# Kernel tuning notes

Measured on AMD Instinct MI355X. Metric: run time of the kernel, lower is better.

The kernel has to match this reference:

```python
import jax, jax.numpy as jnp
import numpy as np
from jax import lax

MINUS_INF = -1.0e9
BOS, EOS, PAD = 0, 1, 2
NB_LABELS, MAX_DEPTH, EXTRA = 96, 8, 3
STATE = NB_LABELS * MAX_DEPTH + EXTRA  # 771
B, T = 32, 128


def _init_transitions(key):
    t = jax.random.uniform(key, (STATE, STATE), minval=-0.1, maxval=0.1, dtype=jnp.float32)
    # structural constraints from init_weights()
    t = t.at[:, BOS].set(MINUS_INF)          # nothing transitions into BOS
    t = t.at[EOS, :].set(MINUS_INF)          # nothing leaves EOS
    t = t.at[BOS, NB_LABELS + EXTRA:].set(MINUS_INF)  # BOS only into depth-0 states
    t = t.at[NB_LABELS + EXTRA:, EOS].set(MINUS_INF)  # only depth-0 states into EOS
    t = t.at[PAD, :].set(MINUS_INF)
    t = t.at[NB_LABELS + EXTRA:, PAD].set(MINUS_INF)
    t = t.at[PAD, EOS].set(0.0)
    t = t.at[PAD, PAD].set(0.0)
    return t


def setup_inputs() -> dict:
    key = jax.random.key(0)
    k1, k2, k3 = jax.random.split(key, 3)
    emissions = jax.random.normal(k1, (B, T, STATE), dtype=jnp.float32)
    # valid (non-special) states only, so gold-path scores stay finite
    tags = jax.random.randint(k2, (B, T), EXTRA, STATE, dtype=jnp.int64)
    mask = jnp.ones((B, T), dtype=jnp.float32)
    transitions = _init_transitions(k3)
    return {"emissions": emissions, "tags": tags, "mask": mask, "transitions": transitions}


def _crf_nll(emissions, tags, mask, transitions):
    b, t, s = emissions.shape
    tags = tags.astype(jnp.int32)
    batch_idx = jnp.arange(b)

    # ---- gold path score ----
    first = tags[:, 0]
    scores = transitions[BOS, first] + emissions[batch_idx, 0, first]
    prev, cur = tags[:, :-1], tags[:, 1:]
    e_sc = jnp.take_along_axis(emissions[:, 1:], cur[..., None], axis=2)[..., 0]  # (B,T-1)
    t_sc = transitions[prev, cur]                                                 # (B,T-1)
    scores = scores + jnp.sum((e_sc + t_sc) * mask[:, 1:], axis=1)
    last_idx = mask.sum(axis=1).astype(jnp.int32) - 1
    last_tags = tags[batch_idx, last_idx]
    scores = scores + transitions[last_tags, EOS]

    # ---- log partition: forward algorithm (logsumexp DP over S x S) ----
    alphas0 = transitions[BOS][None, :] + emissions[:, 0]  # (B,S)

    def step(alphas, inp):
        em, m = inp  # em: (B,S), m: (B,)
        # (B,S_prev,1) + (S_prev,S_cur) + (B,1,S_cur) -> logsumexp over S_prev
        new = jax.scipy.special.logsumexp(
            alphas[:, :, None] + transitions[None, :, :] + em[:, None, :], axis=1)
        alphas = jnp.where(m[:, None] > 0, new, alphas)
        return alphas, None

    alphas, _ = lax.scan(step, alphas0,
                         (jnp.swapaxes(emissions[:, 1:], 0, 1), mask[:, 1:].T))
    log_z = jax.scipy.special.logsumexp(alphas + transitions[:, EOS][None, :], axis=1)

    # nll = -sum(score - logZ)
    return -jnp.sum(scores - log_z)


def reference(emissions, tags, mask, transitions):
    return _crf_nll(emissions, tags, mask, transitions)
```

## Files before the change

kernel.cpp:

```cpp
#include <hip/hip_runtime.h>
#include <math.h>

typedef unsigned long long u64;

static constexpr int S    = 771;
static constexpr int Tn   = 128;
static constexpr int Bn   = 32;
static constexpr int BOSs = 0;
static constexpr int EOSs = 1;

static constexpr int JPAD  = 832;
static constexpr int JB    = 13;
static constexpr int ROWS  = 64;
static constexpr int NQ    = 4;
static constexpr int SL    = JPAD / NQ;
static constexpr int CH    = SL / 16;
static constexpr int EBLK  = NQ * CH * ROWS * 16;
static constexpr int ETOT  = JB * EBLK;
static constexpr int XSTR  = 224;
static constexpr float CB  = 8.0f;
static constexpr float C0V = 4.5f;

__device__ __forceinline__ float wave_max_bfly(float v) {
    #pragma unroll
    for (int off = 32; off > 0; off >>= 1) v = fmaxf(v, __shfl_xor(v, off));
    return v;
}
__device__ __forceinline__ float wave_sum_f(float v) {
    #pragma unroll
    for (int off = 32; off > 0; off >>= 1) v += __shfl_down(v, off);
    return v;
}

__device__ __forceinline__ u64 ald64(const u64* p) {
    return __hip_atomic_load((u64*)p, __ATOMIC_RELAXED, __HIP_MEMORY_SCOPE_AGENT);
}
__device__ __forceinline__ void ast64(u64* p, u64 v) {
    __hip_atomic_store(p, v, __ATOMIC_RELAXED, __HIP_MEMORY_SCOPE_AGENT);
}
__device__ __forceinline__ u64 pack(unsigned tag, unsigned payload) {
    return ((u64)tag << 32) | (u64)payload;
}

#if __has_builtin(__builtin_amdgcn_sdot4)
__device__ __forceinline__ int dot4i(unsigned a, unsigned b, int c) {
    return __builtin_amdgcn_sdot4((int)a, (int)b, c, false);
}
#else
__device__ __forceinline__ int dot4i(unsigned a, unsigned b, int c) {
    c += (int)(a & 0xff)         * (int)(b & 0xff);
    c += (int)((a >> 8) & 0xff)  * (int)((b >> 8) & 0xff);
    c += (int)((a >> 16) & 0xff) * (int)((b >> 16) & 0xff);
    c += (int)((a >> 24) & 0xff) * (int)((b >> 24) & 0xff);
    return c;
}
#endif

extern "C" __global__ void build_tabs(const float* __restrict__ trans,
                                      unsigned char* __restrict__ eswz,
                                      float* __restrict__ eteos) {
    int idx = blockIdx.x * blockDim.x + threadIdx.x;
    if (idx < JPAD)
        eteos[idx] = (idx < S) ? __expf(trans[idx * S + EOSs]) : 0.f;
    if (idx >= ETOT) return;
    int e = idx & 15;
    int q = idx >> 4;
    int lane = q & 63;  q >>= 6;
    int kk = q % 13;
    int h  = q / 13;
    int w  = h & 3, jblk = h >> 2;
    int i = w * SL + kk * 16 + e;
    int j = jblk * ROWS + lane;
    float v = 0.f;
    if (i < S && j < S) v = 115.f * __expf(trans[i * S + j]);
    int q8 = (int)(v + 0.5f);
    if (q8 > 127) q8 = 127;
    eswz[idx] = (unsigned char)q8;
}

__device__ __forceinline__ void publish(u64* W, int jblk, unsigned tag,
                                        float af, float C, int lane) {
    float xf = fminf(127.f, 127.f * __expf(af - C));
    int xi = (int)(xf + 0.5f);
    int b0 = __shfl(xi, (4 * lane) & 63);
    int b1 = __shfl(xi, (4 * lane + 1) & 63);
    int b2 = __shfl(xi, (4 * lane + 2) & 63);
    int b3 = __shfl(xi, (4 * lane + 3) & 63);
    unsigned payload = (unsigned)b0 | ((unsigned)b1 << 8)
                     | ((unsigned)b2 << 16) | ((unsigned)b3 << 24);
    float mc = wave_max_bfly(af);
    u64* base = W + 17 * jblk;
    if (lane < 16)  ast64(base + lane, pack(tag, payload));
    if (lane == 16) ast64(base + 16,   pack(tag, __float_as_uint(mc)));
}

extern "C" __global__ __launch_bounds__(256, 2)
void crf_fwd(const float* __restrict__ em, const float* __restrict__ mask,
             const float* __restrict__ trans, const int* __restrict__ tags,
             const unsigned char* __restrict__ eswz,
             const float* __restrict__ eteos,
             u64* __restrict__ xb, float* __restrict__ out) {
    const int jblk = blockIdx.x, b = blockIdx.y;
    const int tid = threadIdx.x, lane = tid & 63, w = tid >> 6;
    const int j0 = jblk * ROWS;
    const int bw = (13 * w) / 4;
    const int lo = 52 * w - 16 * bw;

    __shared__ __align__(16) unsigned char Elds[EBLK];
    __shared__ __align__(16) unsigned pq[NQ][SL / 4];
    __shared__ int   part[2][NQ][ROWS];
    __shared__ float cshare;
    __shared__ float redv[4], redm[4];

    const float KLOG  = __logf(115.f * 127.f);
    const float KL127 = __logf(127.f);

    {
        const unsigned char* gsrc = eswz + (size_t)jblk * EBLK;
        #pragma unroll
        for (int it = 0; it < EBLK / 4096; ++it)
            *(float4*)(Elds + it * 4096 + tid * 16) =
                *(const float4*)(gsrc + it * 4096 + tid * 16);
    }

    float af = -INFINITY, Cuse = C0V;
    if (w == 0) {
        int j = j0 + lane;
        if (j < S) af = trans[BOSs * S + j] + em[((size_t)b * Tn + 0) * S + j];
        publish(xb + ((size_t)0 * Bn + b) * XSTR, jblk, 0u, af, C0V, lane);
    }

    const bool pollmax = (w == 0) && (lane < JB);

    for (int t = 1; t < Tn; ++t) {
        const u64* R = xb + ((size_t)((t - 1) & 1) * Bn + b) * XSTR;
        u64*       W = xb + ((size_t)((t    ) & 1) * Bn + b) * XSTR;

        float emv = 0.f, mval = 0.f;
        if (w == 0) {
            const int j = j0 + lane;
            if (j < S) emv = em[((size_t)b * Tn + t) * S + j];
            mval = mask[b * Tn + t];
        }

        const unsigned tg = (unsigned)(t - 1);
        const u64* pd = R + 17 * (bw + (lane >> 4)) + (lane & 15);
        const u64* pm = R + 17 * lane + 16;
        u64 qd = 0, qm = 0;
        bool okd = false, okm = !pollmax;
        do {
            if (!okd) { qd = ald64(pd); okd = ((unsigned)(qd >> 32) == tg); }
            if (!okm) { qm = ald64(pm); okm = ((unsigned)(qm >> 32) == tg); }
        } while (__any((!okd) | (!okm)));

        if (lane >= lo && lane < lo + 52) pq[w][lane - lo] = (unsigned)qd;

        float Cnew = 0.f;
        if (w == 0) {
            float mv = (lane < JB) ? __uint_as_float((unsigned)qm) : -INFINITY;
            Cnew = wave_max_bfly(mv) + CB;
        }

        int acc = 0;
        const uint4* E4 = (const uint4*)Elds;
        const uint4* P4 = (const uint4*)pq[w];
        #pragma unroll
        for (int kk = 0; kk < CH; ++kk) {
            const uint4 ev = E4[(w * CH + kk) * 64 + lane];
            const uint4 pv = P4[kk];
            acc = dot4i(ev.x, pv.x, acc);
            acc = dot4i(ev.y, pv.y, acc);
            acc = dot4i(ev.z, pv.z, acc);
            acc = dot4i(ev.w, pv.w, acc);
        }
        part[t & 1][w][lane] = acc;
        __syncthreads();

        if (w == 0) {
            int s4 = part[t & 1][0][lane] + part[t & 1][1][lane]
                   + part[t & 1][2][lane] + part[t & 1][3][lane];
            float nv = Cuse - KLOG + __logf((float)s4) + emv;
            af = (mval > 0.f) ? nv : af;
            publish(W, jblk, (unsigned)t, af, Cnew, lane);
            if (lane == 0) cshare = Cnew;
            Cuse = Cnew;
        }
    }

    if (jblk == 0) {
        const u64* R = xb + ((size_t)((Tn - 1) & 1) * Bn + b) * XSTR;
        const unsigned tg = (unsigned)(Tn - 1);
        const bool act = (tid < JB * 16);
        u64 q = 0;
        bool ok = !act;
        while (true) {
            if (!ok) {
                q = ald64(R + 17 * (tid >> 4) + (tid & 15));
                ok = ((unsigned)(q >> 32) == tg);
            }
            if (__syncthreads_and(ok)) break;
        }
        float lsum = 0.f;
        if (act) {
            unsigned pv = (unsigned)q;
            int base = 4 * tid;
            lsum = (float)(pv & 0xff)         * eteos[base]
                 + (float)((pv >> 8)  & 0xff) * eteos[base + 1]
                 + (float)((pv >> 16) & 0xff) * eteos[base + 2]
                 + (float)((pv >> 24) & 0xff) * eteos[base + 3];
        }
        float mk = 0.f, val = 0.f;
        if (tid < Tn) {
            mk = mask[b * Tn + tid];
            if (tid > 0) {
                int cur  = tags[b * Tn + tid];
                int prev = tags[b * Tn + tid - 1];
                val = (em[((size_t)b * Tn + tid) * S + cur]
                       + trans[prev * S + cur]) * mk;
            }
        }
        lsum = wave_sum_f(lsum);
        float vs = wave_sum_f(val);
        float ms = wave_sum_f(mk);
        if (lane == 0) { redv[w] = vs; redm[w] = ms; part[0][0][w] = 0; }
        if (lane == 1) part[1][0][w] = __float_as_int(lsum);
        __syncthreads();
        if (tid == 0) {
            float tot = __int_as_float(part[1][0][0]) + __int_as_float(part[1][0][1])
                      + __int_as_float(part[1][0][2]) + __int_as_float(part[1][0][3]);
            float logz = cshare - KL127 + __logf(tot);
            float msum = redm[0] + redm[1] + redm[2] + redm[3];
            int last   = (int)(msum + 0.5f) - 1;
            int first  = tags[b * Tn];
            int lastt  = tags[b * Tn + last];
            float score = redv[0] + redv[1] + redv[2] + redv[3]
                        + trans[BOSs * S + first]
                        + em[((size_t)b * Tn) * S + first]
                        + trans[lastt * S + EOSs];
            atomicAdd(out, -(score - logz));
        }
    }
}

extern "C" void kernel_launch(void* const* d_in, const int* in_sizes, int n_in,
                              void* d_out, int out_size, void* d_ws, size_t ws_size,
                              hipStream_t stream) {
    const float* em    = (const float*)d_in[0];
    const int*   tags  = (const int*)d_in[1];
    const float* mask  = (const float*)d_in[2];
    const float* trans = (const float*)d_in[3];
    float* out = (float*)d_out;

    char* ws = (char*)d_ws;
    size_t off = 0;
    unsigned char* eswz = (unsigned char*)(ws + off);
    off += (size_t)ETOT;
    off = (off + 255) & ~(size_t)255;
    float* eteos = (float*)(ws + off); off += JPAD * sizeof(float);
    off = (off + 255) & ~(size_t)255;
    u64* xb = (u64*)(ws + off);        off += (size_t)2 * Bn * XSTR * sizeof(u64);

    (void)hipMemsetAsync(out, 0, sizeof(float), stream);

    build_tabs<<<(ETOT + 255) / 256, 256, 0, stream>>>(trans, eswz, eteos);
    crf_fwd<<<dim3(JB, Bn), 256, 0, stream>>>(em, mask, trans, tags, eswz,
                                              eteos, xb, out);
}
```

Before: 391.0 us.

## Add L2-scoped fast polling path with epoch tags and XCD-aware block mapping

Publishes each step's quantized alpha payload twice: once with sc0 stores to a fast buffer meant to be polled through L2, and once with agent-scope atomics to a fallback buffer. Consumers spin on the fast buffer with sc0 loads up to a cap, then fall back to the coherent buffer for the rest of the run. Tags now carry a per-launch epoch read from s_memrealtime, so stale data from earlier launches cannot be mistaken for fresh data. Blocks are remapped from a 2D grid to a 1D index so that the 13 blocks of one batch row share an XCD. The aim is lower cross-block handoff latency, at the cost of doubled stores, reliance on L2 coherence that only holds within one XCD, and a global epoch handshake at start.

After: 501.0 us. +28.1%, slower.

```diff
diff --git a/kernel.cpp b/kernel.cpp
--- a/kernel.cpp
+++ b/kernel.cpp
@@ -18,6 +18,7 @@
 static constexpr int EBLK  = NQ * CH * ROWS * 16;
 static constexpr int ETOT  = JB * EBLK;
 static constexpr int XSTR  = 224;
+static constexpr int CAP   = 512;
 static constexpr float CB  = 8.0f;
 static constexpr float C0V = 4.5f;
 
@@ -37,6 +38,17 @@
 }
 __device__ __forceinline__ void ast64(u64* p, u64 v) {
     __hip_atomic_store(p, v, __ATOMIC_RELAXED, __HIP_MEMORY_SCOPE_AGENT);
+}
+__device__ __forceinline__ void ld2_l2(const u64* p0, const u64* p1,
+                                       u64& a, u64& c) {
+    asm volatile("global_load_dwordx2 %0, %2, off sc0\n\t"
+                 "global_load_dwordx2 %1, %3, off sc0\n\t"
+                 "s_waitcnt vmcnt(0)"
+                 : "=&v"(a), "=&v"(c) : "v"(p0), "v"(p1) : "memory");
+}
+__device__ __forceinline__ void st_l2(u64* p, u64 v) {
+    asm volatile("global_store_dwordx2 %0, %1, off sc0"
+                 :: "v"(p), "v"(v) : "memory");
 }
 __device__ __forceinline__ u64 pack(unsigned tag, unsigned payload) {
     return ((u64)tag << 32) | (u64)payload;
@@ -78,8 +90,9 @@
     eswz[idx] = (unsigned char)q8;
 }
 
-__device__ __forceinline__ void publish(u64* W, int jblk, unsigned tag,
-                                        float af, float C, int lane) {
+__device__ __forceinline__ void publish2(u64* WF, u64* WM, int jblk,
+                                         unsigned tag, float af, float C,
+                                         int lane) {
     float xf = fminf(127.f, 127.f * __expf(af - C));
     int xi = (int)(xf + 0.5f);
     int b0 = __shfl(xi, (4 * lane) & 63);
@@ -89,9 +102,12 @@
     unsigned payload = (unsigned)b0 | ((unsigned)b1 << 8)
                      | ((unsigned)b2 << 16) | ((unsigned)b3 << 24);
     float mc = wave_max_bfly(af);
-    u64* base = W + 17 * jblk;
-    if (lane < 16)  ast64(base + lane, pack(tag, payload));
-    if (lane == 16) ast64(base + 16,   pack(tag, __float_as_uint(mc)));
+    u64 vd = pack(tag, payload);
+    u64 vm = pack(tag, __float_as_uint(mc));
+    u64* bF = WF + 17 * jblk;
+    u64* bM = WM + 17 * jblk;
+    if (lane < 16)  { st_l2(bF + lane, vd); ast64(bM + lane, vd); }
+    if (lane == 16) { st_l2(bF + 16, vm);   ast64(bM + 16, vm); }
 }
 
 extern "C" __global__ __launch_bounds__(256, 2)
@@ -99,8 +115,11 @@
              const float* __restrict__ trans, const int* __restrict__ tags,
              const unsigned char* __restrict__ eswz,
              const float* __restrict__ eteos,
-             u64* __restrict__ xb, float* __restrict__ out) {
-    const int jblk = blockIdx.x, b = blockIdx.y;
+             u64* __restrict__ xbF, u64* __restrict__ xbM,
+             unsigned* __restrict__ ctl, float* __restrict__ out) {
+    const int l = blockIdx.x;
+    const int b    = (l & 7) + 8 * ((l >> 3) / JB);
+    const int jblk = (l >> 3) % JB;
     const int tid = threadIdx.x, lane = tid & 63, w = tid >> 6;
     const int j0 = jblk * ROWS;
     const int bw = (13 * w) / 4;
@@ -111,6 +130,7 @@
     __shared__ int   part[2][NQ][ROWS];
     __shared__ float cshare;
     __shared__ float redv[4], redm[4];
+    __shared__ unsigned sh_ep;
 
     const float KLOG  = __logf(115.f * 127.f);
     const float KL127 = __logf(127.f);
@@ -123,18 +143,39 @@
                 *(const float4*)(gsrc + it * 4096 + tid * 16);
     }
 
+    if (l == 0 && tid == 0) {
+        u64 rt;
+        asm volatile("s_memrealtime %0\n\ts_waitcnt lgkmcnt(0)" : "=s"(rt));
+        unsigned ep = ((unsigned)rt & 0xffffff00u) | 1u;
+        __hip_atomic_store(ctl, ep, __ATOMIC_RELAXED, __HIP_MEMORY_SCOPE_AGENT);
+    }
+    if (tid == 0) {
+        unsigned ev;
+        do {
+            ev = __hip_atomic_load(ctl, __ATOMIC_RELAXED,
+                                   __HIP_MEMORY_SCOPE_AGENT);
+        } while (!(ev & 1u));
+        sh_ep = ev;
+    }
+    __syncthreads();
+    const unsigned epoch = sh_ep;
+
     float af = -INFINITY, Cuse = C0V;
     if (w == 0) {
         int j = j0 + lane;
         if (j < S) af = trans[BOSs * S + j] + em[((size_t)b * Tn + 0) * S + j];
-        publish(xb + ((size_t)0 * Bn + b) * XSTR, jblk, 0u, af, C0V, lane);
+        publish2(xbF + ((size_t)0 * Bn + b) * XSTR,
+                 xbM + ((size_t)0 * Bn + b) * XSTR, jblk, epoch, af, C0V, lane);
     }
 
     const bool pollmax = (w == 0) && (lane < JB);
+    bool tryfast = true;
 
     for (int t = 1; t < Tn; ++t) {
-        const u64* R = xb + ((size_t)((t - 1) & 1) * Bn + b) * XSTR;
-        u64*       W = xb + ((size_t)((t    ) & 1) * Bn + b) * XSTR;
+        const size_t ro = ((size_t)((t - 1) & 1) * Bn + b) * XSTR;
+        const size_t wo = ((size_t)((t    ) & 1) * Bn + b) * XSTR;
+        const u64* RF = xbF + ro;
+        const u64* RM = xbM + ro;
 
         float emv = 0.f, mval = 0.f;
         if (w == 0) {
@@ -143,15 +184,32 @@
             mval = mask[b * Tn + t];
         }
 
-        const unsigned tg = (unsigned)(t - 1);
-        const u64* pd = R + 17 * (bw + (lane >> 4)) + (lane & 15);
-        const u64* pm = R + 17 * lane + 16;
+        const unsigned tg = epoch + (unsigned)(t - 1);
+        const int doff = 17 * (bw + (lane >> 4)) + (lane & 15);
+        const int moff = 17 * (pollmax ? lane : 0) + 16;
         u64 qd = 0, qm = 0;
         bool okd = false, okm = !pollmax;
-        do {
-            if (!okd) { qd = ald64(pd); okd = ((unsigned)(qd >> 32) == tg); }
-            if (!okm) { qm = ald64(pm); okm = ((unsigned)(qm >> 32) == tg); }
-        } while (__any((!okd) | (!okm)));
+        if (tryfast) {
+            const u64* pdF = RF + doff;
+            const u64* pmF = RF + moff;
+            int spins = 0;
+            for (;;) {
+                u64 a, c;
+                ld2_l2(pdF, pmF, a, c);
+                if (!okd) { qd = a; okd = ((unsigned)(qd >> 32) == tg); }
+                if (!okm) { qm = c; okm = ((unsigned)(qm >> 32) == tg); }
+                if (!__any((!okd) | (!okm))) break;
+                if (++spins >= CAP) { tryfast = false; break; }
+            }
+        }
+        if (__any((!okd) | (!okm))) {
+            const u64* pdM = RM + doff;
+            const u64* pmM = RM + moff;
+            do {
+                if (!okd) { qd = ald64(pdM); okd = ((unsigned)(qd >> 32) == tg); }
+                if (!okm) { qm = ald64(pmM); okm = ((unsigned)(qm >> 32) == tg); }
+            } while (__any((!okd) | (!okm)));
+        }
 
         if (lane >= lo && lane < lo + 52) pq[w][lane - lo] = (unsigned)qd;
 
@@ -181,23 +239,22 @@
                    + part[t & 1][2][lane] + part[t & 1][3][lane];
             float nv = Cuse - KLOG + __logf((float)s4) + emv;
             af = (mval > 0.f) ? nv : af;
-            publish(W, jblk, (unsigned)t, af, Cnew, lane);
+            publish2(xbF + wo, xbM + wo, jblk, epoch + (unsigned)t,
+                     af, Cnew, lane);
             if (lane == 0) cshare = Cnew;
             Cuse = Cnew;
         }
     }
 
     if (jblk == 0) {
-        const u64* R = xb + ((size_t)((Tn - 1) & 1) * Bn + b) * XSTR;
-        const unsigned tg = (unsigned)(Tn - 1);
+        const u64* R = xbM + ((size_t)((Tn - 1) & 1) * Bn + b) * XSTR;
+        const unsigned tg = epoch + (unsigned)(Tn - 1);
         const bool act = (tid < JB * 16);
+        const u64* pp = R + 17 * (tid >> 4) + (tid & 15);
         u64 q = 0;
         bool ok = !act;
         while (true) {
-            if (!ok) {
-                q = ald64(R + 17 * (tid >> 4) + (tid & 15));
-                ok = ((unsigned)(q >> 32) == tg);
-            }
+            if (!ok) { q = ald64(pp); ok = ((unsigned)(q >> 32) == tg); }
             if (__syncthreads_and(ok)) break;
         }
         float lsum = 0.f;
@@ -258,11 +315,15 @@
     off = (off + 255) & ~(size_t)255;
     float* eteos = (float*)(ws + off); off += JPAD * sizeof(float);
     off = (off + 255) & ~(size_t)255;
-    u64* xb = (u64*)(ws + off);        off += (size_t)2 * Bn * XSTR * sizeof(u64);
+    u64* xbF = (u64*)(ws + off);       off += (size_t)2 * Bn * XSTR * sizeof(u64);
+    off = (off + 255) & ~(size_t)255;
+    u64* xbM = (u64*)(ws + off);       off += (size_t)2 * Bn * XSTR * sizeof(u64);
+    off = (off + 255) & ~(size_t)255;
+    unsigned* ctl = (unsigned*)(ws + off); off += 256;
 
     (void)hipMemsetAsync(out, 0, sizeof(float), stream);
 
     build_tabs<<<(ETOT + 255) / 256, 256, 0, stream>>>(trans, eswz, eteos);
-    crf_fwd<<<dim3(JB, Bn), 256, 0, stream>>>(em, mask, trans, tags, eswz,
-                                              eteos, xb, out);
-}
+    crf_fwd<<<dim3(JB * Bn), 256, 0, stream>>>(em, mask, trans, tags, eswz,
+                                               eteos, xbF, xbM, ctl, out);
+}
```

## Process two batch rows per block and embed fp16 max in each published word

Applied to the files above, without the earlier changes.

Each workgroup now handles two sequences, interleaving their recurrence steps so one sequence's cross-block exchange latency can overlap the other's dot-product work. The grid is halved, so each block's LDS-resident quantized transition slice is reused for both sequences. The separate per-block max slot is removed: a half-precision running max and a 16-bit tag are packed into every published 64-bit word, so readers get the scale from the same load instead of an extra poll. The costs are reduced precision on the max (fp16), more serialized work per block, and the loss of the global-max poll being done by a single wave.

Result: slower. 435.4 us (+11.3%).

```diff
diff --git a/kernel.cpp b/kernel.cpp
--- a/kernel.cpp
+++ b/kernel.cpp
@@ -17,7 +17,9 @@
 static constexpr int CH    = SL / 16;
 static constexpr int EBLK  = NQ * CH * ROWS * 16;
 static constexpr int ETOT  = JB * EBLK;
+static constexpr int NPUB  = 16;
 static constexpr int XSTR  = 224;
+static constexpr unsigned TAGB = 0x5A00u;
 static constexpr float CB  = 8.0f;
 static constexpr float C0V = 4.5f;
 
@@ -32,14 +34,13 @@
     return v;
 }
 
+union HU16 { _Float16 h; unsigned short u; };
+
 __device__ __forceinline__ u64 ald64(const u64* p) {
     return __hip_atomic_load((u64*)p, __ATOMIC_RELAXED, __HIP_MEMORY_SCOPE_AGENT);
 }
 __device__ __forceinline__ void ast64(u64* p, u64 v) {
     __hip_atomic_store(p, v, __ATOMIC_RELAXED, __HIP_MEMORY_SCOPE_AGENT);
-}
-__device__ __forceinline__ u64 pack(unsigned tag, unsigned payload) {
-    return ((u64)tag << 32) | (u64)payload;
 }
 
 #if __has_builtin(__builtin_amdgcn_sdot4)
@@ -78,20 +79,20 @@
     eswz[idx] = (unsigned char)q8;
 }
 
-__device__ __forceinline__ void publish(u64* W, int jblk, unsigned tag,
-                                        float af, float C, int lane) {
+__device__ __forceinline__ void publish(u64* base, unsigned tg, float af,
+                                        float C, int lane) {
     float xf = fminf(127.f, 127.f * __expf(af - C));
     int xi = (int)(xf + 0.5f);
-    int b0 = __shfl(xi, (4 * lane) & 63);
-    int b1 = __shfl(xi, (4 * lane + 1) & 63);
-    int b2 = __shfl(xi, (4 * lane + 2) & 63);
-    int b3 = __shfl(xi, (4 * lane + 3) & 63);
-    unsigned payload = (unsigned)b0 | ((unsigned)b1 << 8)
-                     | ((unsigned)b2 << 16) | ((unsigned)b3 << 24);
+    int c0 = __shfl(xi, (4 * lane) & 63);
+    int c1 = __shfl(xi, (4 * lane + 1) & 63);
+    int c2 = __shfl(xi, (4 * lane + 2) & 63);
+    int c3 = __shfl(xi, (4 * lane + 3) & 63);
+    unsigned payload = (unsigned)c0 | ((unsigned)c1 << 8)
+                     | ((unsigned)c2 << 16) | ((unsigned)c3 << 24);
     float mc = wave_max_bfly(af);
-    u64* base = W + 17 * jblk;
-    if (lane < 16)  ast64(base + lane, pack(tag, payload));
-    if (lane == 16) ast64(base + 16,   pack(tag, __float_as_uint(mc)));
+    HU16 hh; hh.h = (_Float16)mc;
+    u64 v = ((u64)tg << 48) | ((u64)hh.u << 32) | (u64)payload;
+    if (lane < NPUB) ast64(base + lane, v);
 }
 
 extern "C" __global__ __launch_bounds__(256, 2)
@@ -100,16 +101,19 @@
              const unsigned char* __restrict__ eswz,
              const float* __restrict__ eteos,
              u64* __restrict__ xb, float* __restrict__ out) {
-    const int jblk = blockIdx.x, b = blockIdx.y;
+    const int jblk = blockIdx.x;
+    const int b0 = blockIdx.y * 2, b1 = b0 + 1;
     const int tid = threadIdx.x, lane = tid & 63, w = tid >> 6;
     const int j0 = jblk * ROWS;
     const int bw = (13 * w) / 4;
     const int lo = 52 * w - 16 * bw;
 
     __shared__ __align__(16) unsigned char Elds[EBLK];
-    __shared__ __align__(16) unsigned pq[NQ][SL / 4];
+    __shared__ __align__(16) unsigned pq[2][NQ][52];
     __shared__ int   part[2][NQ][ROWS];
-    __shared__ float cshare;
+    __shared__ float wmax[2][NQ];
+    __shared__ float csh[2];
+    __shared__ float lz[2][4];
     __shared__ float redv[4], redm[4];
 
     const float KLOG  = __logf(115.f * 127.f);
@@ -123,121 +127,159 @@
                 *(const float4*)(gsrc + it * 4096 + tid * 16);
     }
 
+    const int myb = (w == 1) ? b1 : b0;
     float af = -INFINITY, Cuse = C0V;
-    if (w == 0) {
+    if (w < 2) {
         int j = j0 + lane;
-        if (j < S) af = trans[BOSs * S + j] + em[((size_t)b * Tn + 0) * S + j];
-        publish(xb + ((size_t)0 * Bn + b) * XSTR, jblk, 0u, af, C0V, lane);
+        if (j < S) af = trans[BOSs * S + j] + em[((size_t)myb * Tn + 0) * S + j];
+        publish(xb + ((size_t)0 * Bn + myb) * XSTR + NPUB * jblk,
+                TAGB | 0u, af, C0V, lane);
     }
 
-    const bool pollmax = (w == 0) && (lane < JB);
-
     for (int t = 1; t < Tn; ++t) {
-        const u64* R = xb + ((size_t)((t - 1) & 1) * Bn + b) * XSTR;
-        u64*       W = xb + ((size_t)((t    ) & 1) * Bn + b) * XSTR;
+        const unsigned tgp = TAGB | (unsigned)(t - 1);
+        const unsigned tgc = TAGB | (unsigned)t;
 
         float emv = 0.f, mval = 0.f;
-        if (w == 0) {
+        if (w < 2) {
             const int j = j0 + lane;
-            if (j < S) emv = em[((size_t)b * Tn + t) * S + j];
-            mval = mask[b * Tn + t];
-        }
-
-        const unsigned tg = (unsigned)(t - 1);
-        const u64* pd = R + 17 * (bw + (lane >> 4)) + (lane & 15);
-        const u64* pm = R + 17 * lane + 16;
-        u64 qd = 0, qm = 0;
-        bool okd = false, okm = !pollmax;
-        do {
-            if (!okd) { qd = ald64(pd); okd = ((unsigned)(qd >> 32) == tg); }
-            if (!okm) { qm = ald64(pm); okm = ((unsigned)(qm >> 32) == tg); }
-        } while (__any((!okd) | (!okm)));
-
-        if (lane >= lo && lane < lo + 52) pq[w][lane - lo] = (unsigned)qd;
-
-        float Cnew = 0.f;
-        if (w == 0) {
-            float mv = (lane < JB) ? __uint_as_float((unsigned)qm) : -INFINITY;
-            Cnew = wave_max_bfly(mv) + CB;
-        }
-
-        int acc = 0;
-        const uint4* E4 = (const uint4*)Elds;
-        const uint4* P4 = (const uint4*)pq[w];
-        #pragma unroll
-        for (int kk = 0; kk < CH; ++kk) {
-            const uint4 ev = E4[(w * CH + kk) * 64 + lane];
-            const uint4 pv = P4[kk];
-            acc = dot4i(ev.x, pv.x, acc);
-            acc = dot4i(ev.y, pv.y, acc);
-            acc = dot4i(ev.z, pv.z, acc);
-            acc = dot4i(ev.w, pv.w, acc);
-        }
-        part[t & 1][w][lane] = acc;
-        __syncthreads();
-
-        if (w == 0) {
-            int s4 = part[t & 1][0][lane] + part[t & 1][1][lane]
-                   + part[t & 1][2][lane] + part[t & 1][3][lane];
-            float nv = Cuse - KLOG + __logf((float)s4) + emv;
-            af = (mval > 0.f) ? nv : af;
-            publish(W, jblk, (unsigned)t, af, Cnew, lane);
-            if (lane == 0) cshare = Cnew;
-            Cuse = Cnew;
+            if (j < S) emv = em[((size_t)myb * Tn + t) * S + j];
+            mval = mask[myb * Tn + t];
+        }
+
+        {
+            const u64* R = xb + ((size_t)((t - 1) & 1) * Bn + b0) * XSTR;
+            const u64* pd = R + NPUB * (bw + (lane >> 4)) + (lane & 15);
+            u64 q = 0; bool ok = false;
+            do {
+                if (!ok) { q = ald64(pd); ok = ((unsigned)(q >> 48) == tgp); }
+            } while (__any(!ok));
+            if (lane >= lo && lane < lo + 52) pq[0][w][lane - lo] = (unsigned)q;
+            HU16 hm; hm.u = (unsigned short)(q >> 32);
+            float wm = wave_max_bfly((float)hm.h);
+            if (lane == 0) wmax[0][w] = wm;
+
+            int acc = 0;
+            const uint4* E4 = (const uint4*)Elds;
+            const uint4* P4 = (const uint4*)pq[0][w];
+            #pragma unroll
+            for (int kk = 0; kk < CH; ++kk) {
+                const uint4 ev = E4[(w * CH + kk) * 64 + lane];
+                const uint4 pv = P4[kk];
+                acc = dot4i(ev.x, pv.x, acc); acc = dot4i(ev.y, pv.y, acc);
+                acc = dot4i(ev.z, pv.z, acc); acc = dot4i(ev.w, pv.w, acc);
+            }
+            part[0][w][lane] = acc;
+            __syncthreads();
+            if (w == 0) {
+                int s4 = part[0][0][lane] + part[0][1][lane]
+                       + part[0][2][lane] + part[0][3][lane];
+                float Cnew = fmaxf(fmaxf(wmax[0][0], wmax[0][1]),
+                                   fmaxf(wmax[0][2], wmax[0][3])) + CB;
+                float nv = Cuse - KLOG + __logf((float)s4) + emv;
+                af = (mval > 0.f) ? nv : af;
+                publish(xb + ((size_t)(t & 1) * Bn + b0) * XSTR + NPUB * jblk,
+                        tgc, af, Cnew, lane);
+                Cuse = Cnew;
+            }
+        }
+
+        {
+            const u64* R = xb + ((size_t)((t - 1) & 1) * Bn + b1) * XSTR;
+            const u64* pd = R + NPUB * (bw + (lane >> 4)) + (lane & 15);
+            u64 q = 0; bool ok = false;
+            do {
+                if (!ok) { q = ald64(pd); ok = ((unsigned)(q >> 48) == tgp); }
+            } while (__any(!ok));
+            if (lane >= lo && lane < lo + 52) pq[1][w][lane - lo] = (unsigned)q;
+            HU16 hm; hm.u = (unsigned short)(q >> 32);
+            float wm = wave_max_bfly((float)hm.h);
+            if (lane == 0) wmax[1][w] = wm;
+
+            int acc = 0;
+            const uint4* E4 = (const uint4*)Elds;
+            const uint4* P4 = (const uint4*)pq[1][w];
+            #pragma unroll
+            for (int kk = 0; kk < CH; ++kk) {
+                const uint4 ev = E4[(w * CH + kk) * 64 + lane];
+                const uint4 pv = P4[kk];
+                acc = dot4i(ev.x, pv.x, acc); acc = dot4i(ev.y, pv.y, acc);
+                acc = dot4i(ev.z, pv.z, acc); acc = dot4i(ev.w, pv.w, acc);
+            }
+            part[1][w][lane] = acc;
+            __syncthreads();
+            if (w == 1) {
+                int s4 = part[1][0][lane] + part[1][1][lane]
+                       + part[1][2][lane] + part[1][3][lane];
+                float Cnew = fmaxf(fmaxf(wmax[1][0], wmax[1][1]),
+                                   fmaxf(wmax[1][2], wmax[1][3])) + CB;
+                float nv = Cuse - KLOG + __logf((float)s4) + emv;
+                af = (mval > 0.f) ? nv : af;
+                publish(xb + ((size_t)(t & 1) * Bn + b1) * XSTR + NPUB * jblk,
+                        tgc, af, Cnew, lane);
+                Cuse = Cnew;
+            }
         }
     }
 
     if (jblk == 0) {
-        const u64* R = xb + ((size_t)((Tn - 1) & 1) * Bn + b) * XSTR;
-        const unsigned tg = (unsigned)(Tn - 1);
-        const bool act = (tid < JB * 16);
-        u64 q = 0;
-        bool ok = !act;
+        if (w < 2 && lane == 0) csh[w] = Cuse;
+        const unsigned tgf = TAGB | (unsigned)(Tn - 1);
+        const u64* RA = xb + ((size_t)((Tn - 1) & 1) * Bn + b0) * XSTR;
+        const u64* RB = xb + ((size_t)((Tn - 1) & 1) * Bn + b1) * XSTR;
+        const bool actp = (tid < JB * NPUB);
+        u64 qa = 0, qb = 0;
+        bool oka = !actp, okb = !actp;
         while (true) {
-            if (!ok) {
-                q = ald64(R + 17 * (tid >> 4) + (tid & 15));
-                ok = ((unsigned)(q >> 32) == tg);
-            }
-            if (__syncthreads_and(ok)) break;
-        }
-        float lsum = 0.f;
-        if (act) {
-            unsigned pv = (unsigned)q;
+            if (!oka) { qa = ald64(RA + tid); oka = ((unsigned)(qa >> 48) == tgf); }
+            if (!okb) { qb = ald64(RB + tid); okb = ((unsigned)(qb >> 48) == tgf); }
+            if (__syncthreads_and(oka & okb)) break;
+        }
+        float lA = 0.f, lB = 0.f;
+        if (actp) {
+            unsigned pa = (unsigned)qa, pb = (unsigned)qb;
             int base = 4 * tid;
-            lsum = (float)(pv & 0xff)         * eteos[base]
-                 + (float)((pv >> 8)  & 0xff) * eteos[base + 1]
-                 + (float)((pv >> 16) & 0xff) * eteos[base + 2]
-                 + (float)((pv >> 24) & 0xff) * eteos[base + 3];
-        }
-        float mk = 0.f, val = 0.f;
-        if (tid < Tn) {
-            mk = mask[b * Tn + tid];
-            if (tid > 0) {
-                int cur  = tags[b * Tn + tid];
-                int prev = tags[b * Tn + tid - 1];
-                val = (em[((size_t)b * Tn + tid) * S + cur]
-                       + trans[prev * S + cur]) * mk;
-            }
-        }
-        lsum = wave_sum_f(lsum);
+            lA = (float)(pa & 0xff)         * eteos[base]
+               + (float)((pa >> 8)  & 0xff) * eteos[base + 1]
+               + (float)((pa >> 16) & 0xff) * eteos[base + 2]
+               + (float)((pa >> 24) & 0xff) * eteos[base + 3];
+            lB = (float)(pb & 0xff)         * eteos[base]
+               + (float)((pb >> 8)  & 0xff) * eteos[base + 1]
+               + (float)((pb >> 16) & 0xff) * eteos[base + 2]
+               + (float)((pb >> 24) & 0xff) * eteos[base + 3];
+        }
+        lA = wave_sum_f(lA);
+        lB = wave_sum_f(lB);
+        if (lane == 0) { lz[0][w] = lA; lz[1][w] = lB; }
+
+        int pos = tid & 127;
+        int gb  = (tid < 128) ? b0 : b1;
+        float mk = mask[gb * Tn + pos];
+        float val = 0.f;
+        if (pos > 0) {
+            int cur  = tags[gb * Tn + pos];
+            int prev = tags[gb * Tn + pos - 1];
+            val = (em[((size_t)gb * Tn + pos) * S + cur]
+                   + trans[prev * S + cur]) * mk;
+        }
         float vs = wave_sum_f(val);
         float ms = wave_sum_f(mk);
-        if (lane == 0) { redv[w] = vs; redm[w] = ms; part[0][0][w] = 0; }
-        if (lane == 1) part[1][0][w] = __float_as_int(lsum);
+        if (lane == 0) { redv[w] = vs; redm[w] = ms; }
         __syncthreads();
         if (tid == 0) {
-            float tot = __int_as_float(part[1][0][0]) + __int_as_float(part[1][0][1])
-                      + __int_as_float(part[1][0][2]) + __int_as_float(part[1][0][3]);
-            float logz = cshare - KL127 + __logf(tot);
-            float msum = redm[0] + redm[1] + redm[2] + redm[3];
-            int last   = (int)(msum + 0.5f) - 1;
-            int first  = tags[b * Tn];
-            int lastt  = tags[b * Tn + last];
-            float score = redv[0] + redv[1] + redv[2] + redv[3]
-                        + trans[BOSs * S + first]
-                        + em[((size_t)b * Tn) * S + first]
-                        + trans[lastt * S + EOSs];
-            atomicAdd(out, -(score - logz));
+            float totA = lz[0][0] + lz[0][1] + lz[0][2] + lz[0][3];
+            float totB = lz[1][0] + lz[1][1] + lz[1][2] + lz[1][3];
+            float logzA = csh[0] - KL127 + __logf(totA);
+            float logzB = csh[1] - KL127 + __logf(totB);
+            float msA = redm[0] + redm[1], msB = redm[2] + redm[3];
+            int lastA = (int)(msA + 0.5f) - 1, lastB = (int)(msB + 0.5f) - 1;
+            int fA = tags[b0 * Tn], fB = tags[b1 * Tn];
+            int lTA = tags[b0 * Tn + lastA], lTB = tags[b1 * Tn + lastB];
+            float scoreA = redv[0] + redv[1] + trans[BOSs * S + fA]
+                         + em[((size_t)b0 * Tn) * S + fA] + trans[lTA * S + EOSs];
+            float scoreB = redv[2] + redv[3] + trans[BOSs * S + fB]
+                         + em[((size_t)b1 * Tn) * S + fB] + trans[lTB * S + EOSs];
+            atomicAdd(out, -(scoreA - logzA) - (scoreB - logzB));
         }
     }
 }
@@ -263,6 +305,6 @@
     (void)hipMemsetAsync(out, 0, sizeof(float), stream);
 
     build_tabs<<<(ETOT + 255) / 256, 256, 0, stream>>>(trans, eswz, eteos);
-    crf_fwd<<<dim3(JB, Bn), 256, 0, stream>>>(em, mask, trans, tags, eswz,
-                                              eteos, xb, out);
-}
+    crf_fwd<<<dim3(JB, Bn / 2), 256, 0, stream>>>(em, mask, trans, tags, eswz,
+                                                  eteos, xb, out);
+}
```

## Split rows across waves so each wave publishes independently without block barrier

Applied to the files above, without the earlier changes.

Reassigns work so each of the four waves owns 16 output rows and the full 832-column dot product, reduced with in-wave shuffles instead of an LDS partial-sum exchange and __syncthreads. Each wave now publishes its own 4-word slice with the per-slice max packed as fp16 alongside a 16-bit tag, so the separate max words and their polling disappear. The goal is to shorten the per-timestep critical path of the cross-block recurrence. In exchange every wave polls all 208 words, and the fp16 max and shorter tag lose some precision and range.

Measured after the change: 416.6 us. 1.07x slower.

```diff
diff --git a/kernel.cpp b/kernel.cpp
--- a/kernel.cpp
+++ b/kernel.cpp
@@ -11,13 +11,13 @@
 
 static constexpr int JPAD  = 832;
 static constexpr int JB    = 13;
-static constexpr int ROWS  = 64;
 static constexpr int NQ    = 4;
-static constexpr int SL    = JPAD / NQ;
-static constexpr int CH    = SL / 16;
-static constexpr int EBLK  = NQ * CH * ROWS * 16;
+static constexpr int CH    = 13;
+static constexpr int EBLK  = NQ * CH * 64 * 16;
 static constexpr int ETOT  = JB * EBLK;
-static constexpr int XSTR  = 224;
+static constexpr int WORDS = 208;
+static constexpr int XSTR  = 256;
+static constexpr unsigned TAGB = 0x5A00u;
 static constexpr float CB  = 8.0f;
 static constexpr float C0V = 4.5f;
 
@@ -32,14 +32,13 @@
     return v;
 }
 
+union HU16 { _Float16 h; unsigned short u; };
+
 __device__ __forceinline__ u64 ald64(const u64* p) {
     return __hip_atomic_load((u64*)p, __ATOMIC_RELAXED, __HIP_MEMORY_SCOPE_AGENT);
 }
 __device__ __forceinline__ void ast64(u64* p, u64 v) {
     __hip_atomic_store(p, v, __ATOMIC_RELAXED, __HIP_MEMORY_SCOPE_AGENT);
-}
-__device__ __forceinline__ u64 pack(unsigned tag, unsigned payload) {
-    return ((u64)tag << 32) | (u64)payload;
 }
 
 #if __has_builtin(__builtin_amdgcn_sdot4)
@@ -64,13 +63,14 @@
         eteos[idx] = (idx < S) ? __expf(trans[idx * S + EOSs]) : 0.f;
     if (idx >= ETOT) return;
     int e = idx & 15;
-    int q = idx >> 4;
-    int lane = q & 63;  q >>= 6;
-    int kk = q % 13;
-    int h  = q / 13;
+    int t = idx >> 4;
+    int lane = t & 63;  t >>= 6;
+    int kk = t % 13;
+    int h  = t / 13;
     int w  = h & 3, jblk = h >> 2;
-    int i = w * SL + kk * 16 + e;
-    int j = jblk * ROWS + lane;
+    int q = lane >> 4, r = lane & 15;
+    int i = q * 208 + kk * 16 + e;
+    int j = jblk * 64 + w * 16 + r;
     float v = 0.f;
     if (i < S && j < S) v = 115.f * __expf(trans[i * S + j]);
     int q8 = (int)(v + 0.5f);
@@ -78,20 +78,21 @@
     eswz[idx] = (unsigned char)q8;
 }
 
-__device__ __forceinline__ void publish(u64* W, int jblk, unsigned tag,
-                                        float af, float C, int lane) {
+__device__ __forceinline__ void publish(u64* base, unsigned tg, float af,
+                                        float C, int lane) {
     float xf = fminf(127.f, 127.f * __expf(af - C));
     int xi = (int)(xf + 0.5f);
-    int b0 = __shfl(xi, (4 * lane) & 63);
-    int b1 = __shfl(xi, (4 * lane + 1) & 63);
-    int b2 = __shfl(xi, (4 * lane + 2) & 63);
-    int b3 = __shfl(xi, (4 * lane + 3) & 63);
-    unsigned payload = (unsigned)b0 | ((unsigned)b1 << 8)
-                     | ((unsigned)b2 << 16) | ((unsigned)b3 << 24);
-    float mc = wave_max_bfly(af);
-    u64* base = W + 17 * jblk;
-    if (lane < 16)  ast64(base + lane, pack(tag, payload));
-    if (lane == 16) ast64(base + 16,   pack(tag, __float_as_uint(mc)));
+    float m = (lane < 16) ? af : -INFINITY;
+    m = wave_max_bfly(m);
+    int c0 = __shfl(xi, (4 * lane) & 63);
+    int c1 = __shfl(xi, (4 * lane + 1) & 63);
+    int c2 = __shfl(xi, (4 * lane + 2) & 63);
+    int c3 = __shfl(xi, (4 * lane + 3) & 63);
+    unsigned payload = (unsigned)c0 | ((unsigned)c1 << 8)
+                     | ((unsigned)c2 << 16) | ((unsigned)c3 << 24);
+    HU16 hh; hh.h = (_Float16)m;
+    u64 v = ((u64)tg << 48) | ((u64)hh.u << 32) | (u64)payload;
+    if (lane < 4) ast64(base + lane, v);
 }
 
 extern "C" __global__ __launch_bounds__(256, 2)
@@ -102,14 +103,14 @@
              u64* __restrict__ xb, float* __restrict__ out) {
     const int jblk = blockIdx.x, b = blockIdx.y;
     const int tid = threadIdx.x, lane = tid & 63, w = tid >> 6;
-    const int j0 = jblk * ROWS;
-    const int bw = (13 * w) / 4;
-    const int lo = 52 * w - 16 * bw;
+    const int j0 = jblk * 64;
+    const int q = lane >> 4;
+    const int myrow = j0 + w * 16 + lane;
 
     __shared__ __align__(16) unsigned char Elds[EBLK];
-    __shared__ __align__(16) unsigned pq[NQ][SL / 4];
-    __shared__ int   part[2][NQ][ROWS];
+    __shared__ __align__(16) unsigned pstr[NQ][WORDS];
     __shared__ float cshare;
+    __shared__ float lzred[4];
     __shared__ float redv[4], redm[4];
 
     const float KLOG  = __logf(115.f * 127.f);
@@ -124,85 +125,82 @@
     }
 
     float af = -INFINITY, Cuse = C0V;
-    if (w == 0) {
-        int j = j0 + lane;
-        if (j < S) af = trans[BOSs * S + j] + em[((size_t)b * Tn + 0) * S + j];
-        publish(xb + ((size_t)0 * Bn + b) * XSTR, jblk, 0u, af, C0V, lane);
-    }
-
-    const bool pollmax = (w == 0) && (lane < JB);
+    if (lane < 16 && myrow < S)
+        af = trans[BOSs * S + myrow] + em[((size_t)b * Tn + 0) * S + myrow];
+    publish(xb + ((size_t)0 * Bn + b) * XSTR + (jblk * NQ + w) * 4,
+            TAGB | 0u, af, C0V, lane);
+
+    const bool k3 = (lane < WORDS - 192);
 
     for (int t = 1; t < Tn; ++t) {
         const u64* R = xb + ((size_t)((t - 1) & 1) * Bn + b) * XSTR;
-        u64*       W = xb + ((size_t)((t    ) & 1) * Bn + b) * XSTR;
-
-        float emv = 0.f, mval = 0.f;
-        if (w == 0) {
-            const int j = j0 + lane;
-            if (j < S) emv = em[((size_t)b * Tn + t) * S + j];
-            mval = mask[b * Tn + t];
-        }
-
-        const unsigned tg = (unsigned)(t - 1);
-        const u64* pd = R + 17 * (bw + (lane >> 4)) + (lane & 15);
-        const u64* pm = R + 17 * lane + 16;
-        u64 qd = 0, qm = 0;
-        bool okd = false, okm = !pollmax;
+        u64*       W = xb + ((size_t)((t    ) & 1) * Bn + b) * XSTR
+                          + (jblk * NQ + w) * 4;
+
+        float emv = 0.f;
+        if (lane < 16 && myrow < S)
+            emv = em[((size_t)b * Tn + t) * S + myrow];
+        const float mval = mask[b * Tn + t];
+
+        const unsigned tg = TAGB | (unsigned)(t - 1);
+        u64 q0 = 0, q1 = 0, q2 = 0, q3 = 0;
+        bool o0 = false, o1 = false, o2 = false, o3 = !k3;
         do {
-            if (!okd) { qd = ald64(pd); okd = ((unsigned)(qd >> 32) == tg); }
-            if (!okm) { qm = ald64(pm); okm = ((unsigned)(qm >> 32) == tg); }
-        } while (__any((!okd) | (!okm)));
-
-        if (lane >= lo && lane < lo + 52) pq[w][lane - lo] = (unsigned)qd;
-
-        float Cnew = 0.f;
-        if (w == 0) {
-            float mv = (lane < JB) ? __uint_as_float((unsigned)qm) : -INFINITY;
-            Cnew = wave_max_bfly(mv) + CB;
-        }
+            if (!o0) { q0 = ald64(R + lane);       o0 = ((unsigned)(q0 >> 48) == tg); }
+            if (!o1) { q1 = ald64(R + lane + 64);  o1 = ((unsigned)(q1 >> 48) == tg); }
+            if (!o2) { q2 = ald64(R + lane + 128); o2 = ((unsigned)(q2 >> 48) == tg); }
+            if (!o3) { q3 = ald64(R + lane + 192); o3 = ((unsigned)(q3 >> 48) == tg); }
+        } while (__any((!o0) | (!o1) | (!o2) | (!o3)));
+
+        pstr[w][lane]       = (unsigned)q0;
+        pstr[w][lane + 64]  = (unsigned)q1;
+        pstr[w][lane + 128] = (unsigned)q2;
+        if (k3) pstr[w][lane + 192] = (unsigned)q3;
+
+        HU16 h0, h1, h2, h3;
+        h0.u = (unsigned short)(q0 >> 32);
+        h1.u = (unsigned short)(q1 >> 32);
+        h2.u = (unsigned short)(q2 >> 32);
+        h3.u = (unsigned short)(q3 >> 32);
+        float mx = fmaxf(fmaxf((float)h0.h, (float)h1.h), (float)h2.h);
+        if (k3) mx = fmaxf(mx, (float)h3.h);
+        const float Cnew = wave_max_bfly(mx) + CB;
 
         int acc = 0;
         const uint4* E4 = (const uint4*)Elds;
-        const uint4* P4 = (const uint4*)pq[w];
+        const uint4* P4 = (const uint4*)&pstr[w][52 * q];
         #pragma unroll
         for (int kk = 0; kk < CH; ++kk) {
             const uint4 ev = E4[(w * CH + kk) * 64 + lane];
             const uint4 pv = P4[kk];
-            acc = dot4i(ev.x, pv.x, acc);
-            acc = dot4i(ev.y, pv.y, acc);
-            acc = dot4i(ev.z, pv.z, acc);
-            acc = dot4i(ev.w, pv.w, acc);
-        }
-        part[t & 1][w][lane] = acc;
-        __syncthreads();
-
-        if (w == 0) {
-            int s4 = part[t & 1][0][lane] + part[t & 1][1][lane]
-                   + part[t & 1][2][lane] + part[t & 1][3][lane];
-            float nv = Cuse - KLOG + __logf((float)s4) + emv;
+            acc = dot4i(ev.x, pv.x, acc); acc = dot4i(ev.y, pv.y, acc);
+            acc = dot4i(ev.z, pv.z, acc); acc = dot4i(ev.w, pv.w, acc);
+        }
+        acc += __shfl_down(acc, 32);
+        acc += __shfl_down(acc, 16);
+
+        if (lane < 16) {
+            float nv = Cuse - KLOG + __logf((float)acc) + emv;
             af = (mval > 0.f) ? nv : af;
-            publish(W, jblk, (unsigned)t, af, Cnew, lane);
-            if (lane == 0) cshare = Cnew;
-            Cuse = Cnew;
-        }
+        }
+        publish(W, TAGB | (unsigned)t, af, Cnew, lane);
+        Cuse = Cnew;
     }
 
     if (jblk == 0) {
+        if (tid == 0) cshare = Cuse;
         const u64* R = xb + ((size_t)((Tn - 1) & 1) * Bn + b) * XSTR;
-        const unsigned tg = (unsigned)(Tn - 1);
-        const bool act = (tid < JB * 16);
-        u64 q = 0;
+        const unsigned tgf = TAGB | (unsigned)(Tn - 1);
+        const bool act = (tid < WORDS);
+        u64 qf = 0;
         bool ok = !act;
         while (true) {
-            if (!ok) {
-                q = ald64(R + 17 * (tid >> 4) + (tid & 15));
-                ok = ((unsigned)(q >> 32) == tg);
-            }
+            if (!ok) { qf = ald64(R + tid); ok = ((unsigned)(qf >> 48) == tgf); }
             if (__syncthreads_and(ok)) break;
         }
         float lsum = 0.f;
         if (act) {
-            unsigned pv = (unsigned)q;
+            unsigned pv = (unsigned)qf;
             int base = 4 * tid;
             lsum = (float)(pv & 0xff)         * eteos[base]
                  + (float)((pv >> 8)  & 0xff) * eteos[base + 1]
@@ -222,12 +220,10 @@
         lsum = wave_sum_f(lsum);
         float vs = wave_sum_f(val);
         float ms = wave_sum_f(mk);
-        if (lane == 0) { redv[w] = vs; redm[w] = ms; part[0][0][w] = 0; }
-        if (lane == 1) part[1][0][w] = __float_as_int(lsum);
+        if (lane == 0) { redv[w] = vs; redm[w] = ms; lzred[w] = lsum; }
         __syncthreads();
         if (tid == 0) {
-            float tot = __int_as_float(part[1][0][0]) + __int_as_float(part[1][0][1])
-                      + __int_as_float(part[1][0][2]) + __int_as_float(part[1][0][3]);
+            float tot  = lzred[0] + lzred[1] + lzred[2] + lzred[3];
             float logz = cshare - KL127 + __logf(tot);
             float msum = redm[0] + redm[1] + redm[2] + redm[3];
             int last   = (int)(msum + 0.5f) - 1;
```
